# Kernel optimization log

Hardware: AMD Instinct MI355X
Metric: run time of the kernel (lower is better)

Reference implementation:

```python
import jax, jax.numpy as jnp
import numpy as np

DN = ('NCH', 'OIH', 'NCH')

def conv1d(x, w, b, pad):
    y = jax.lax.conv_general_dilated(x, w, (1,), [(pad, pad)], dimension_numbers=DN)
    return y if b is None else y + b[None, :, None]

def bn_eval(x, g, b, m, v, eps):
    s = g * jax.lax.rsqrt(v + eps)
    return x * s[None, :, None] + (b - m * s)[None, :, None]

def swish(x):
    return x * jax.nn.sigmoid(x)

def setup_inputs() -> dict:
    key = jax.random.key(0)
    ks = jax.random.split(key, 8)
    B, T, P = 16, 8192, 32
    inp = {
        'x': jax.random.normal(ks[0], (B, 1, T), jnp.float32),
        'conv_w': jax.random.normal(ks[1], (512, 1, 9), jnp.float32) * 0.1,
        'bn_g': jnp.ones((512,), jnp.float32),
        'bn_b': jnp.zeros((512,), jnp.float32),
        'bn_m': jnp.zeros((512,), jnp.float32),
        'bn_v': jnp.ones((512,), jnp.float32),
        'p1_w': jax.random.normal(ks[2], (P, 2, 31), jnp.float32) * 0.1,
        'p1_b': jnp.zeros((P,), jnp.float32),
        'pbn1_g': jnp.ones((P,), jnp.float32),
        'pbn1_b': jnp.zeros((P,), jnp.float32),
        'pbn1_m': jnp.zeros((P,), jnp.float32),
        'pbn1_v': jnp.ones((P,), jnp.float32),
        'p2_w': jax.random.normal(ks[3], (P, P, 15), jnp.float32) * 0.05,
        'p2_b': jnp.zeros((P,), jnp.float32),
        'pbn2_g': jnp.ones((P,), jnp.float32),
        'pbn2_b': jnp.zeros((P,), jnp.float32),
        'pbn2_m': jnp.zeros((P,), jnp.float32),
        'pbn2_v': jnp.ones((P,), jnp.float32),
        'p3_w': jax.random.normal(ks[4], (2, P, 15), jnp.float32) * 0.001,  # source scales last conv weight by 0.01
        'p3_b': jnp.full((2,), -np.log(2.0), jnp.float32),                 # source sets bias to -log(2)
        'norm_mean': jnp.ones((1,), jnp.float32),                           # eval-mode renorm buffer
    }
    return inp

def reference(x, conv_w, bn_g, bn_b, bn_m, bn_v,
              p1_w, p1_b, pbn1_g, pbn1_b, pbn1_m, pbn1_v,
              p2_w, p2_b, pbn2_g, pbn2_b, pbn2_m, pbn2_v,
              p3_w, p3_b, norm_mean):
    B, _, T = x.shape
    # main conv -> BN(eps=1e-3) -> GLU(dim=1); dropout is identity in eval
    h = conv1d(x, conv_w, None, 9 // 2)                 # [B, 512, T]
    h = bn_eval(h, bn_g, bn_b, bn_m, bn_v, 1e-3)
    a, g = jnp.split(h, 2, axis=1)
    features = a * jax.nn.sigmoid(g)                    # [B, 256, T]
    # predictor on cat([x, x*x])
    j = conv1d(jnp.concatenate([x, x * x], axis=1), p1_w, p1_b, 15)
    j = swish(bn_eval(j, pbn1_g, pbn1_b, pbn1_m, pbn1_v, 1e-5))
    j = conv1d(j, p2_w, p2_b, 7)
    j = swish(bn_eval(j, pbn2_g, pbn2_b, pbn2_m, pbn2_v, 1e-5))
    j = conv1d(j, p3_w, p3_b, 7)                        # [B, 2, T]
    weights = jax.nn.sigmoid(j[:, 0, :])                # [B, T]
    moves = jax.nn.sigmoid(j[:, 1, :])
    bmoves = moves
    moves = moves * norm_mean[0]                        # eval: renorm = norm_mean buffer
    # CIF-style dynamic pooling (row_pool), vectorized over batch
    feats = jnp.transpose(features, (0, 2, 1))          # [B, T, C]
    fw = feats * weights[..., None]
    poses = jnp.cumsum(jax.lax.stop_gradient(moves), axis=1)  # moves.detach() in source
    floors = jnp.floor(poses)
    w1 = 1.0 - (poses - floors)
    w2 = poses - floors
    fl = floors.astype(jnp.int32)
    ce = fl + 1
    Lmax = T + 2  # static bound: poses <= T so ceil index <= T+1
    C = fw.shape[2]
    def pool(fw_i, fl_i, ce_i, w1_i, w2_i):
        out = jnp.zeros((Lmax, C), fw_i.dtype)
        out = out.at[fl_i].add(w1_i[:, None] * fw_i)
        out = out.at[ce_i].add(w2_i[:, None] * fw_i)
        return out
    x_evs = jax.vmap(pool)(fw, fl, ce, w1, w2)          # [B, Lmax, C]
    lens = fl[:, -1] + 2                                 # int(ceils[-1]) + 1
    x_evs = jnp.transpose(x_evs, (0, 2, 1))             # [B, C, Lmax]
    pad = 3 - (Lmax % 3)
    x_evs = jnp.pad(x_evs, ((0, 0), (0, 0), (0, pad)))
    return x_evs, lens, bmoves, weights
```

## Files before the change

kernel.cpp:

```cpp
#include <hip/hip_runtime.h>
#include <math.h>

static constexpr int TT = 8192;
static constexpr int LFULL = 8196;
static constexpr int BSTRIDE = LFULL + 2;

static constexpr size_t XE_OFF   = 0;
static constexpr size_t LENS_OFF = (size_t)16*256*LFULL;
static constexpr size_t BM_OFF   = LENS_OFF + 16;
static constexpr size_t WT_OFF   = BM_OFF + (size_t)16*TT;

static constexpr size_t U_OFF     = 0;
static constexpr size_t V_OFF     = U_OFF + (size_t)16*32*TT;
static constexpr size_t MOVES_OFF = V_OFF + (size_t)16*32*TT;
static constexpr size_t C1_OFF    = MOVES_OFF + (size_t)16*TT;
static constexpr size_t C2_OFF    = C1_OFF + (size_t)16*TT;
static constexpr size_t BND_OFF   = U_OFF;

__device__ __forceinline__ float sig_(float z) { return 1.0f / (1.0f + __expf(-z)); }

typedef float f4v __attribute__((ext_vector_type(4)));
__device__ __forceinline__ void nt_store4(float* p, float a, float b, float c, float d) {
    f4v v = {a, b, c, d};
    __builtin_nontemporal_store(v, (f4v*)p);
}

static constexpr int US = 304;

__global__ __launch_bounds__(512, 2) void k_convall(
    const float* __restrict__ x,
    const float* __restrict__ p1w, const float* __restrict__ p1b,
    const float* __restrict__ g1, const float* __restrict__ b1,
    const float* __restrict__ m1, const float* __restrict__ v1,
    const float* __restrict__ p2w, const float* __restrict__ p2b,
    const float* __restrict__ g2, const float* __restrict__ b2,
    const float* __restrict__ m2, const float* __restrict__ v2,
    const float* __restrict__ p3w, const float* __restrict__ p3b,
    const float* __restrict__ nm,
    float* __restrict__ outw, float* __restrict__ outbm, float* __restrict__ moves)
{
    __shared__ __align__(16) float xin[320];
    __shared__ __align__(16) float w1t[2 * 992];
    __shared__ __align__(16) float uld[32 * US + 4];
    __shared__ __align__(16) float w2t[32 * 512];
    __shared__ __align__(16) float wsh[960];
    const int tid = threadIdx.x;
    const int b = blockIdx.y;
    const int t0 = blockIdx.x * 256;

    if (tid < 320) {
        int id = t0 - 29 + tid;
        xin[tid] = (id >= 0 && id < TT) ? x[b * TT + id] : 0.f;
    }
#pragma unroll
    for (int it = 0; it < 4; ++it) {
        int idx = it * 512 + tid;
        if (idx < 1984) {
            int c = idx / 62; int r = idx - c * 62; int ci = r / 31; int k = r - ci * 31;
            w1t[ci * 992 + c * 31 + k] = p1w[idx];
        }
    }
#pragma unroll
    for (int it = 0; it < 32; ++it) {
        int idx = it * 512 + tid;
        int ci = idx >> 9; int r = idx & 511; int oc = r >> 4; int k = r & 15;
        int sw = (oc >> 1) & 3;
        int phys = ci * 512 + oc * 16 + ((((k >> 2) ^ sw) << 2) | (k & 3));
        w2t[phys] = (k < 15) ? p2w[oc * 480 + ci * 15 + k] : 0.f;
    }
    if (tid < 512) { if (tid < 960 - 512) wsh[512 + tid] = p3w[512 + tid]; wsh[tid] = p3w[tid]; }
    __syncthreads();

    {
        const int cB = tid & 31, pg = tid >> 5;
        const float s1v = g1[cB] * rsqrtf(v1[cB] + 1e-5f);
        const float sh1 = b1[cB] - m1[cB] * s1v;
        const float bias1 = p1b[cB];
        const int base = pg * 20;
        const float* wA = &w1t[cB * 31];
        const float* wB = &w1t[992 + cB * 31];
#pragma unroll
        for (int h = 0; h < 3; ++h) {
            const int off = h * 8;
            const int len = (h < 2) ? 8 : 4;
            const int nld = (h < 2) ? 10 : 9;
            const int ul0 = base + off;
            if (ul0 < 284) {
                float win[40], wsq[40];
                const float4* xp = (const float4*)(&xin[ul0]);
#pragma unroll
                for (int r = 0; r < 10; ++r) {
                    if (r < nld) {
                        float4 q = xp[r];
                        win[4*r] = q.x; win[4*r+1] = q.y; win[4*r+2] = q.z; win[4*r+3] = q.w;
                    }
                }
#pragma unroll
                for (int i = 0; i < 40; ++i) { if (i < 4 * nld) wsq[i] = win[i] * win[i]; }
                float acc[8];
#pragma unroll
                for (int i = 0; i < 8; ++i) acc[i] = bias1;
#pragma unroll
                for (int k = 0; k < 31; ++k) {
                    const float a = wA[k], bw = wB[k];
#pragma unroll
                    for (int i = 0; i < 8; ++i) {
                        if (i < len) {
                            acc[i] = fmaf(a, win[i + k], acc[i]);
                            acc[i] = fmaf(bw, wsq[i + k], acc[i]);
                        }
                    }
                }
#pragma unroll
                for (int qq = 0; qq < 8; qq += 4) {
                    if (qq < len && ul0 + qq < 284) {
                        f4v ov;
#pragma unroll
                        for (int i = 0; i < 4; ++i) {
                            const float z = fmaf(acc[qq + i], s1v, sh1);
                            ov[i] = z * sig_(z);
                        }
                        *(f4v*)&uld[cB * US + ul0 + qq] = ov;
                    }
                }
            }
        }
    }
    __syncthreads();

    const int cl = tid & 31;
    const int tg = tid >> 5;
    const int swz = ((cl >> 1) & 3) << 2;

    float o[16];
    {
        float acc2[16];
        const float bias2 = p2b[cl];
#pragma unroll
        for (int i = 0; i < 16; ++i) acc2[i] = bias2;
        for (int ci = 0; ci < 32; ++ci) {
            float win[32];
            const float4* wp = (const float4*)(&uld[ci * US + tg * 16]);
#pragma unroll
            for (int r = 0; r < 8; ++r) {
                float4 q = wp[r];
                win[4*r] = q.x; win[4*r+1] = q.y; win[4*r+2] = q.z; win[4*r+3] = q.w;
            }
            float w[16];
            const float* wrow = &w2t[ci * 512 + cl * 16];
#pragma unroll
            for (int r = 0; r < 4; ++r) {
                float4 q = *(const float4*)(&wrow[(4 * r) ^ swz]);
                w[4*r] = q.x; w[4*r+1] = q.y; w[4*r+2] = q.z; w[4*r+3] = q.w;
            }
#pragma unroll
            for (int k = 0; k < 15; ++k)
#pragma unroll
                for (int i = 0; i < 16; ++i) acc2[i] = fmaf(w[k], win[i + k], acc2[i]);
        }
        const float s = g2[cl] * rsqrtf(v2[cl] + 1e-5f);
        const float sh = b2[cl] - m2[cl] * s;
        const int tvb = t0 - 7 + tg * 16;
#pragma unroll
        for (int i = 0; i < 16; ++i) {
            const float z = fmaf(acc2[i], s, sh);
            const float vvv = z * sig_(z);
            const int tv = tvb + i;
            o[i] = (tv >= 0 && tv < TT) ? vvv : 0.f;
        }
    }

    const int lane = tid & 63, wv = tid >> 6;
    const int ocT = ((wv & 1) << 4) + (lane & 15);
    const int sub = lane >> 4;
    const int vl0 = 256 + ((wv >> 1) << 2);
    const int swzT = ((ocT >> 1) & 3) << 2;
    float vt[4];
    {
        float acc4[4] = {0.f, 0.f, 0.f, 0.f};
#pragma unroll
        for (int j = 0; j < 8; ++j) {
            const int ci = sub + 4 * j;
            float win[20];
            const float4* wp = (const float4*)(&uld[ci * US + vl0]);
#pragma unroll
            for (int r = 0; r < 5; ++r) {
                float4 q = wp[r];
                win[4*r] = q.x; win[4*r+1] = q.y; win[4*r+2] = q.z; win[4*r+3] = q.w;
            }
            float w[16];
            const float* wrow = &w2t[ci * 512 + ocT * 16];
#pragma unroll
            for (int r = 0; r < 4; ++r) {
                float4 q = *(const float4*)(&wrow[(4 * r) ^ swzT]);
                w[4*r] = q.x; w[4*r+1] = q.y; w[4*r+2] = q.z; w[4*r+3] = q.w;
            }
#pragma unroll
            for (int k = 0; k < 15; ++k)
#pragma unroll
                for (int i = 0; i < 4; ++i) acc4[i] = fmaf(w[k], win[i + k], acc4[i]);
        }
#pragma unroll
        for (int i = 0; i < 4; ++i) {
            acc4[i] += __shfl_xor(acc4[i], 16, 64);
            acc4[i] += __shfl_xor(acc4[i], 32, 64);
        }
        const float sT = g2[ocT] * rsqrtf(v2[ocT] + 1e-5f);
        const float shT = b2[ocT] - m2[ocT] * sT;
        const float bT = p2b[ocT];
#pragma unroll
        for (int i = 0; i < 4; ++i) {
            const float z = fmaf(acc4[i] + bT, sT, shT);
            const float vvv = z * sig_(z);
            const int tv = t0 - 7 + vl0 + i;
            vt[i] = (tv >= 0 && tv < TT) ? vvv : 0.f;
        }
    }
    __syncthreads();

    {
        float* vbuf = uld;
#pragma unroll
        for (int r = 0; r < 4; ++r) {
            f4v a = {o[4*r], o[4*r+1], o[4*r+2], o[4*r+3]};
            *(f4v*)&vbuf[cl * US + tg * 16 + 4 * r] = a;
        }
        if (sub == 0) {
            f4v a = {vt[0], vt[1], vt[2], vt[3]};
            *(f4v*)&vbuf[ocT * US + vl0] = a;
        }
    }
    __syncthreads();

    {
        const float* vbuf = uld;
        const int g = tid >> 3;
        const int q3 = tid & 7;
        float acc[8];
#pragma unroll
        for (int i = 0; i < 8; ++i) acc[i] = 0.f;
#pragma unroll
        for (int i = 0; i < 4; ++i) {
            const int ci = q3 + 8 * i;
            float win[20];
            const float4* wp = (const float4*)(&vbuf[ci * US + g * 4]);
#pragma unroll
            for (int r = 0; r < 5; ++r) {
                float4 v4 = wp[r];
                win[4*r] = v4.x; win[4*r+1] = v4.y; win[4*r+2] = v4.z; win[4*r+3] = v4.w;
            }
            const float* w0 = &wsh[ci * 15];
            const float* w1p = &wsh[480 + ci * 15];
#pragma unroll
            for (int k = 0; k < 15; ++k) {
                const float a = w0[k], gw = w1p[k];
#pragma unroll
                for (int t4 = 0; t4 < 4; ++t4) {
                    acc[t4]     = fmaf(a,  win[k + t4], acc[t4]);
                    acc[4 + t4] = fmaf(gw, win[k + t4], acc[4 + t4]);
                }
            }
        }
#pragma unroll
        for (int i = 0; i < 8; ++i) {
            acc[i] += __shfl_xor(acc[i], 1, 64);
            acc[i] += __shfl_xor(acc[i], 2, 64);
            acc[i] += __shfl_xor(acc[i], 4, 64);
        }
        if (q3 == 0) {
            const float nmv = nm[0];
            const float b0 = p3b[0], b1v = p3b[1];
            const int t = t0 + g * 4;
            float4 wvv = make_float4(sig_(acc[0]+b0), sig_(acc[1]+b0), sig_(acc[2]+b0), sig_(acc[3]+b0));
            float4 bm = make_float4(sig_(acc[4]+b1v), sig_(acc[5]+b1v), sig_(acc[6]+b1v), sig_(acc[7]+b1v));
            float4 mv = make_float4(bm.x*nmv, bm.y*nmv, bm.z*nmv, bm.w*nmv);
            *(float4*)&outw[b * TT + t]  = wvv;
            *(float4*)&outbm[b * TT + t] = bm;
            *(float4*)&moves[b * TT + t] = mv;
        }
    }
}

__global__ __launch_bounds__(1024) void k_scan(
    const float* __restrict__ moves, const float* __restrict__ wts,
    float* __restrict__ coef1, float* __restrict__ coef2,
    int* __restrict__ bnd, float* __restrict__ lens)
{
    __shared__ float wsum[16];
    const int tid = threadIdx.x;
    const int b = blockIdx.x;
    const int lane = tid & 63, wv = tid >> 6;
    float carry = 0.f;

    int* bb = &bnd[b * BSTRIDE];
    for (int i = tid; i < BSTRIDE; i += 1024) bb[i] = TT;
    if (tid == 0) { bb[0] = 0; bb[1] = 0; }
    __syncthreads();

    const float4* mv4 = (const float4*)&moves[b * TT];
    const float4* wt4 = (const float4*)&wts[b * TT];
    float4* c14 = (float4*)&coef1[b * TT];
    float4* c24 = (float4*)&coef2[b * TT];

    for (int chunk = 0; chunk < 2; ++chunk) {
        const int idx = chunk * 1024 + tid;
        float4 m = mv4[idx];
        const float s = m.x + m.y + m.z + m.w;
        float v = s;
#pragma unroll
        for (int off = 1; off < 64; off <<= 1) {
            float n = __shfl_up(v, off, 64);
            if (lane >= off) v += n;
        }
        if (lane == 63) wsum[wv] = v;
        __syncthreads();
        float pre = carry;
        for (int w = 0; w < wv; ++w) pre += wsum[w];
        float tot = 0.f;
#pragma unroll
        for (int w = 0; w < 16; ++w) tot += wsum[w];
        const float base = pre + (v - s);
        const float p0 = base + m.x;
        const float p1 = p0 + m.y;
        const float p2 = p1 + m.z;
        const float p3 = p2 + m.w;
        const float4 w4 = wt4[idx];
        const float fr0 = p0 - floorf(p0), fr1 = p1 - floorf(p1);
        const float fr2 = p2 - floorf(p2), fr3 = p3 - floorf(p3);
        c14[idx] = make_float4((1.f - fr0) * w4.x, (1.f - fr1) * w4.y,
                               (1.f - fr2) * w4.z, (1.f - fr3) * w4.w);
        c24[idx] = make_float4(fr0 * w4.x, fr1 * w4.y, fr2 * w4.z, fr3 * w4.w);
        {
            int lf = (int)floorf(base) + 1;
            const int lfe = (int)floorf(p3);
            const int tbase = idx << 2;
            for (; lf <= lfe; ++lf) {
                const float lff = (float)lf;
                int t = tbase;
                if (p0 >= lff) { }
                else if (p1 >= lff) t += 1;
                else if (p2 >= lff) t += 2;
                else t += 3;
                if (lf + 1 < BSTRIDE) bb[lf + 1] = t;
            }
        }
        if (chunk == 1 && tid == 1023) lens[b] = floorf(p3) + 2.0f;
        carry += tot;
        __syncthreads();
    }
}

static constexpr int LTILE = 32;
static constexpr int CHK = 256;
static constexpr int NPOOLX = (LFULL + LTILE - 1) / LTILE;

__global__ __launch_bounds__(256) void k_pool(
    const float* __restrict__ x,
    const float* __restrict__ cw,
    const float* __restrict__ bng, const float* __restrict__ bnb,
    const float* __restrict__ bnm, const float* __restrict__ bnv,
    const float* __restrict__ coef1, const float* __restrict__ coef2,
    const int* __restrict__ bnd, const float* __restrict__ lens,
    float* __restrict__ xevs)
{
    __shared__ float out_lds[256 * 33];
    __shared__ float4 xl4[68];
    __shared__ float4 c1l4[CHK / 4], c2l4[CHK / 4];
    __shared__ int lbs[LTILE + 2];
    float* xl = (float*)xl4;
    float* c1l = (float*)c1l4;
    float* c2l = (float*)c2l4;

    const int tid = threadIdx.x;
    const int b = blockIdx.y;

    if (blockIdx.x >= NPOOLX) {
        const int zx = blockIdx.x - NPOOLX;
        const int zs = (((int)lens[b]) + 15) & ~15;
        if (zs >= LFULL) return;
        const int n4 = (LFULL - zs) >> 2;
        for (int r = 0; r < 4; ++r) {
            float* row = &xevs[((size_t)(b * 256 + zx * 4 + r)) * LFULL + zs];
            for (int i = tid; i < n4; i += 256) nt_store4(row + 4 * i, 0.f, 0.f, 0.f, 0.f);
        }
        return;
    }

    const int l0 = blockIdx.x * LTILE;
    const int LTa = min(LTILE, LFULL - l0);

    if (tid < LTa + 2) lbs[tid] = bnd[b * BSTRIDE + l0 + tid];
    __syncthreads();

    const int t_lo = lbs[0];
    const int t_hi = lbs[LTa + 1];
    if (t_lo >= t_hi) return;

    const size_t rowbase = (size_t)b * 256 * LFULL + l0;

#pragma unroll
    for (int li = 0; li < 33; ++li) out_lds[tid * 33 + li] = 0.f;

    const int c = tid;
    float wa[9], wg[9];
#pragma unroll
    for (int k = 0; k < 9; ++k) { wa[k] = cw[c * 9 + k]; wg[k] = cw[(c + 256) * 9 + k]; }
    const float sa = bng[c] * rsqrtf(bnv[c] + 1e-3f);
    const float sha = bnb[c] - bnm[c] * sa;
    const float sg = bng[c + 256] * rsqrtf(bnv[c + 256] + 1e-3f);
    const float shg = bnb[c + 256] - bnm[c + 256] * sg;

    const float* xg = &x[b * TT];
    const float* c1g = &coef1[b * TT];
    const float* c2g = &coef2[b * TT];

    float accA = 0.f, accB = 0.f;
    int j = 0;
    int nb = lbs[1];

    for (int cs = t_lo; cs < t_hi; cs += CHK) {
        const int ce = min(cs + CHK, t_hi);
        const int len = ce - cs;
        __syncthreads();
        for (int idx = tid; idx < len + 12; idx += 256) {
            int id = cs - 4 + idx;
            xl[idx] = (id >= 0 && id < TT) ? xg[id] : 0.f;
        }
        if (tid < len) { c1l[tid] = c1g[cs + tid]; c2l[tid] = c2g[cs + tid]; }
        __syncthreads();

        const int len4 = len >> 2;
        for (int g = 0; g < len4; ++g) {
            float4 A = xl4[g], Bq = xl4[g + 1], Cq = xl4[g + 2];
            float w[12] = {A.x, A.y, A.z, A.w, Bq.x, Bq.y, Bq.z, Bq.w, Cq.x, Cq.y, Cq.z, Cq.w};
            float f[4];
#pragma unroll
            for (int i = 0; i < 4; ++i) {
                float s0 = 0.f, s1 = 0.f;
#pragma unroll
                for (int k = 0; k < 9; ++k) { s0 = fmaf(wa[k], w[i + k], s0); s1 = fmaf(wg[k], w[i + k], s1); }
                const float av = fmaf(s0, sa, sha);
                const float gv = fmaf(s1, sg, shg);
                f[i] = av * sig_(gv);
            }
            float4 c1v = c1l4[g], c2v = c2l4[g];
            const float c1a[4] = {c1v.x, c1v.y, c1v.z, c1v.w};
            const float c2a[4] = {c2v.x, c2v.y, c2v.z, c2v.w};
            const int tb = cs + (g << 2);
#pragma unroll
            for (int i = 0; i < 4; ++i) {
                const int t = tb + i;
                while (t >= nb) {
                    int li = j - 1;
                    if (li >= 0 && li < LTa) out_lds[c * 33 + li] = accA;
                    accA = accB; accB = 0.f;
                    ++j;
                    nb = lbs[j + 1];
                }
                accA = fmaf(c1a[i], f[i], accA);
                accB = fmaf(c2a[i], f[i], accB);
            }
        }
        for (int t = cs + (len4 << 2); t < ce; ++t) {
            const int il = t - cs;
            float s0 = 0.f, s1 = 0.f;
#pragma unroll
            for (int k = 0; k < 9; ++k) { float xv = xl[il + k]; s0 = fmaf(wa[k], xv, s0); s1 = fmaf(wg[k], xv, s1); }
            const float av = fmaf(s0, sa, sha);
            const float gv = fmaf(s1, sg, shg);
            const float f0 = av * sig_(gv);
            while (t >= nb) {
                int li = j - 1;
                if (li >= 0 && li < LTa) out_lds[c * 33 + li] = accA;
                accA = accB; accB = 0.f;
                ++j;
                nb = lbs[j + 1];
            }
            accA = fmaf(c1l[il], f0, accA);
            accB = fmaf(c2l[il], f0, accB);
        }
    }
    {
        int li = j - 1;
        if (li >= 0 && li < LTa) out_lds[c * 33 + li] = accA;
    }
    __syncthreads();

#pragma unroll
    for (int it = 0; it < 8; ++it) {
        int idx4 = it * 256 + tid;
        int cc = idx4 >> 3, q = (idx4 & 7) << 2;
        if (q < LTa) {
            nt_store4(&xevs[rowbase + (size_t)cc * LFULL + q],
                      out_lds[cc * 33 + q + 0], out_lds[cc * 33 + q + 1],
                      out_lds[cc * 33 + q + 2], out_lds[cc * 33 + q + 3]);
        }
    }
}

extern "C" void kernel_launch(void* const* d_in, const int* in_sizes, int n_in,
                              void* d_out, int out_size, void* d_ws, size_t ws_size,
                              hipStream_t stream) {
    (void)in_sizes; (void)n_in; (void)out_size; (void)ws_size;
    const float* x      = (const float*)d_in[0];
    const float* conv_w = (const float*)d_in[1];
    const float* bn_g   = (const float*)d_in[2];
    const float* bn_b   = (const float*)d_in[3];
    const float* bn_m   = (const float*)d_in[4];
    const float* bn_v   = (const float*)d_in[5];
    const float* p1_w   = (const float*)d_in[6];
    const float* p1_b   = (const float*)d_in[7];
    const float* pbn1_g = (const float*)d_in[8];
    const float* pbn1_b = (const float*)d_in[9];
    const float* pbn1_m = (const float*)d_in[10];
    const float* pbn1_v = (const float*)d_in[11];
    const float* p2_w   = (const float*)d_in[12];
    const float* p2_b   = (const float*)d_in[13];
    const float* pbn2_g = (const float*)d_in[14];
    const float* pbn2_b = (const float*)d_in[15];
    const float* pbn2_m = (const float*)d_in[16];
    const float* pbn2_v = (const float*)d_in[17];
    const float* p3_w   = (const float*)d_in[18];
    const float* p3_b   = (const float*)d_in[19];
    const float* nm     = (const float*)d_in[20];

    float* out = (float*)d_out;
    float* ws  = (float*)d_ws;
    float* moves = ws + MOVES_OFF;
    float* coef1 = ws + C1_OFF;
    float* coef2 = ws + C2_OFF;
    int*   bnd   = (int*)(ws + BND_OFF);
    float* xevs  = out + XE_OFF;
    float* lens  = out + LENS_OFF;
    float* bmv   = out + BM_OFF;
    float* wts   = out + WT_OFF;

    k_convall<<<dim3(32, 16), 512, 0, stream>>>(
        x, p1_w, p1_b, pbn1_g, pbn1_b, pbn1_m, pbn1_v,
        p2_w, p2_b, pbn2_g, pbn2_b, pbn2_m, pbn2_v,
        p3_w, p3_b, nm, wts, bmv, moves);
    k_scan<<<16, 1024, 0, stream>>>(moves, wts, coef1, coef2, bnd, lens);
    k_pool<<<dim3(NPOOLX + 64, 16), 256, 0, stream>>>(
        x, conv_w, bn_g, bn_b, bn_m, bn_v, coef1, coef2, bnd, lens, xevs);
}
```

Baseline: 318.8 us.

## Interleave channel pairs in LDS to use packed FP32 FMA for conv2

Rearranges the conv1 output LDS buffer so each pair of input channels is interleaved along time, and reorders the conv2 weights to match with a new XOR swizzle. The conv2 inner loops then work on 2-wide float vectors with elementwise FMA, so the compiler can emit packed FP32 FMAs (v_pk_fma_f32) that handle two channels per instruction. Partial sums from the two channel lanes are added at the end. The third-stage buffer gets its own smaller stride. In exchange, conv1 now writes scalar strided stores instead of vector stores, and more window values stay live in registers, which may raise register pressure.

```diff
diff --git a/kernel.cpp b/kernel.cpp
--- a/kernel.cpp
+++ b/kernel.cpp
@@ -20,12 +20,14 @@
 __device__ __forceinline__ float sig_(float z) { return 1.0f / (1.0f + __expf(-z)); }
 
 typedef float f4v __attribute__((ext_vector_type(4)));
+typedef float f2v __attribute__((ext_vector_type(2)));
 __device__ __forceinline__ void nt_store4(float* p, float a, float b, float c, float d) {
     f4v v = {a, b, c, d};
     __builtin_nontemporal_store(v, (f4v*)p);
 }
 
-static constexpr int US = 304;
+static constexpr int UPS = 572;
+static constexpr int VS  = 276;
 
 __global__ __launch_bounds__(512, 2) void k_convall(
     const float* __restrict__ x,
@@ -41,8 +43,8 @@
 {
     __shared__ __align__(16) float xin[320];
     __shared__ __align__(16) float w1t[2 * 992];
-    __shared__ __align__(16) float uld[32 * US + 4];
-    __shared__ __align__(16) float w2t[32 * 512];
+    __shared__ __align__(16) float uld[16 * UPS + 4];
+    __shared__ __align__(16) float w2t[16 * 1024];
     __shared__ __align__(16) float wsh[960];
     const int tid = threadIdx.x;
     const int b = blockIdx.y;
@@ -63,12 +65,13 @@
 #pragma unroll
     for (int it = 0; it < 32; ++it) {
         int idx = it * 512 + tid;
-        int ci = idx >> 9; int r = idx & 511; int oc = r >> 4; int k = r & 15;
-        int sw = (oc >> 1) & 3;
-        int phys = ci * 512 + oc * 16 + ((((k >> 2) ^ sw) << 2) | (k & 3));
-        w2t[phys] = (k < 15) ? p2w[oc * 480 + ci * 15 + k] : 0.f;
-    }
-    if (tid < 512) { if (tid < 960 - 512) wsh[512 + tid] = p3w[512 + tid]; wsh[tid] = p3w[tid]; }
+        int p = idx >> 10; int r = idx & 1023; int oc = r >> 5; int m = r & 31;
+        int k = m >> 1, par = m & 1;
+        float val = (k < 15) ? p2w[oc * 480 + (2 * p + par) * 15 + k] : 0.f;
+        int phys = (p << 10) + (oc << 5) + ((((m >> 2) ^ (oc & 7)) << 2) | (m & 3));
+        w2t[phys] = val;
+    }
+    { if (tid < 960 - 512) wsh[512 + tid] = p3w[512 + tid]; if (tid < 512) wsh[tid] = p3w[tid]; }
     __syncthreads();
 
     {
@@ -79,6 +82,7 @@
         const int base = pg * 20;
         const float* wA = &w1t[cB * 31];
         const float* wB = &w1t[992 + cB * 31];
+        float* urow = &uld[(cB >> 1) * UPS + (cB & 1)];
 #pragma unroll
         for (int h = 0; h < 3; ++h) {
             const int off = h * 8;
@@ -112,15 +116,10 @@
                     }
                 }
 #pragma unroll
-                for (int qq = 0; qq < 8; qq += 4) {
-                    if (qq < len && ul0 + qq < 284) {
-                        f4v ov;
-#pragma unroll
-                        for (int i = 0; i < 4; ++i) {
-                            const float z = fmaf(acc[qq + i], s1v, sh1);
-                            ov[i] = z * sig_(z);
-                        }
-                        *(f4v*)&uld[cB * US + ul0 + qq] = ov;
+                for (int i = 0; i < 8; ++i) {
+                    if (i < len && ul0 + i < 284) {
+                        const float z = fmaf(acc[i], s1v, sh1);
+                        urow[(ul0 + i) * 2] = z * sig_(z);
                     }
                 }
             }
@@ -130,40 +129,43 @@
 
     const int cl = tid & 31;
     const int tg = tid >> 5;
-    const int swz = ((cl >> 1) & 3) << 2;
 
     float o[16];
     {
-        float acc2[16];
+        f2v accP[16];
+#pragma unroll
+        for (int i = 0; i < 16; ++i) accP[i] = f2v{0.f, 0.f};
+        for (int p = 0; p < 16; ++p) {
+            f2v win2[32];
+            const float4* wp = (const float4*)(&uld[p * UPS + tg * 32]);
+#pragma unroll
+            for (int r = 0; r < 16; ++r) {
+                float4 q = wp[r];
+                win2[2*r]   = f2v{q.x, q.y};
+                win2[2*r+1] = f2v{q.z, q.w};
+            }
+            f2v w2f[16];
+            const float* wrow = &w2t[(p << 10) + (cl << 5)];
+#pragma unroll
+            for (int r = 0; r < 8; ++r) {
+                float4 q = *(const float4*)(&wrow[((r ^ (cl & 7)) << 2)]);
+                w2f[2*r]   = f2v{q.x, q.y};
+                w2f[2*r+1] = f2v{q.z, q.w};
+            }
+#pragma unroll
+            for (int k = 0; k < 15; ++k)
+#pragma unroll
+                for (int i = 0; i < 16; ++i)
+                    accP[i] = __builtin_elementwise_fma(win2[i + k], w2f[k], accP[i]);
+        }
         const float bias2 = p2b[cl];
-#pragma unroll
-        for (int i = 0; i < 16; ++i) acc2[i] = bias2;
-        for (int ci = 0; ci < 32; ++ci) {
-            float win[32];
-            const float4* wp = (const float4*)(&uld[ci * US + tg * 16]);
-#pragma unroll
-            for (int r = 0; r < 8; ++r) {
-                float4 q = wp[r];
-                win[4*r] = q.x; win[4*r+1] = q.y; win[4*r+2] = q.z; win[4*r+3] = q.w;
-            }
-            float w[16];
-            const float* wrow = &w2t[ci * 512 + cl * 16];
-#pragma unroll
-            for (int r = 0; r < 4; ++r) {
-                float4 q = *(const float4*)(&wrow[(4 * r) ^ swz]);
-                w[4*r] = q.x; w[4*r+1] = q.y; w[4*r+2] = q.z; w[4*r+3] = q.w;
-            }
-#pragma unroll
-            for (int k = 0; k < 15; ++k)
-#pragma unroll
-                for (int i = 0; i < 16; ++i) acc2[i] = fmaf(w[k], win[i + k], acc2[i]);
-        }
         const float s = g2[cl] * rsqrtf(v2[cl] + 1e-5f);
         const float sh = b2[cl] - m2[cl] * s;
         const int tvb = t0 - 7 + tg * 16;
 #pragma unroll
         for (int i = 0; i < 16; ++i) {
-            const float z = fmaf(acc2[i], s, sh);
+            const float a2 = accP[i].x + accP[i].y + bias2;
+            const float z = fmaf(a2, s, sh);
             const float vvv = z * sig_(z);
             const int tv = tvb + i;
             o[i] = (tv >= 0 && tv < TT) ? vvv : 0.f;
@@ -174,32 +176,39 @@
     const int ocT = ((wv & 1) << 4) + (lane & 15);
     const int sub = lane >> 4;
     const int vl0 = 256 + ((wv >> 1) << 2);
-    const int swzT = ((ocT >> 1) & 3) << 2;
     float vt[4];
     {
-        float acc4[4] = {0.f, 0.f, 0.f, 0.f};
-#pragma unroll
-        for (int j = 0; j < 8; ++j) {
-            const int ci = sub + 4 * j;
-            float win[20];
-            const float4* wp = (const float4*)(&uld[ci * US + vl0]);
-#pragma unroll
-            for (int r = 0; r < 5; ++r) {
+        f2v accT[4];
+#pragma unroll
+        for (int i = 0; i < 4; ++i) accT[i] = f2v{0.f, 0.f};
+#pragma unroll
+        for (int j = 0; j < 4; ++j) {
+            const int p = sub + 4 * j;
+            f2v win2[20];
+            const float4* wp = (const float4*)(&uld[p * UPS + vl0 * 2]);
+#pragma unroll
+            for (int r = 0; r < 10; ++r) {
                 float4 q = wp[r];
-                win[4*r] = q.x; win[4*r+1] = q.y; win[4*r+2] = q.z; win[4*r+3] = q.w;
-            }
-            float w[16];
-            const float* wrow = &w2t[ci * 512 + ocT * 16];
-#pragma unroll
-            for (int r = 0; r < 4; ++r) {
-                float4 q = *(const float4*)(&wrow[(4 * r) ^ swzT]);
-                w[4*r] = q.x; w[4*r+1] = q.y; w[4*r+2] = q.z; w[4*r+3] = q.w;
+                win2[2*r]   = f2v{q.x, q.y};
+                win2[2*r+1] = f2v{q.z, q.w};
+            }
+            f2v w2f[16];
+            const float* wrow = &w2t[(p << 10) + (ocT << 5)];
+#pragma unroll
+            for (int r = 0; r < 8; ++r) {
+                float4 q = *(const float4*)(&wrow[((r ^ (ocT & 7)) << 2)]);
+                w2f[2*r]   = f2v{q.x, q.y};
+                w2f[2*r+1] = f2v{q.z, q.w};
             }
 #pragma unroll
             for (int k = 0; k < 15; ++k)
 #pragma unroll
-                for (int i = 0; i < 4; ++i) acc4[i] = fmaf(w[k], win[i + k], acc4[i]);
-        }
+                for (int i = 0; i < 4; ++i)
+                    accT[i] = __builtin_elementwise_fma(win2[i + k], w2f[k], accT[i]);
+        }
+        float acc4[4];
+#pragma unroll
+        for (int i = 0; i < 4; ++i) acc4[i] = accT[i].x + accT[i].y;
 #pragma unroll
         for (int i = 0; i < 4; ++i) {
             acc4[i] += __shfl_xor(acc4[i], 16, 64);
@@ -223,11 +232,11 @@
 #pragma unroll
         for (int r = 0; r < 4; ++r) {
             f4v a = {o[4*r], o[4*r+1], o[4*r+2], o[4*r+3]};
-            *(f4v*)&vbuf[cl * US + tg * 16 + 4 * r] = a;
+            *(f4v*)&vbuf[cl * VS + tg * 16 + 4 * r] = a;
         }
         if (sub == 0) {
             f4v a = {vt[0], vt[1], vt[2], vt[3]};
-            *(f4v*)&vbuf[ocT * US + vl0] = a;
+            *(f4v*)&vbuf[ocT * VS + vl0] = a;
         }
     }
     __syncthreads();
@@ -243,7 +252,7 @@
         for (int i = 0; i < 4; ++i) {
             const int ci = q3 + 8 * i;
             float win[20];
-            const float4* wp = (const float4*)(&vbuf[ci * US + g * 4]);
+            const float4* wp = (const float4*)(&vbuf[ci * VS + g * 4]);
 #pragma unroll
             for (int r = 0; r < 5; ++r) {
                 float4 v4 = wp[r];
```

After: 312.0 us. 1.02x faster.
